# Performance work log

Measured on AMD Instinct MI355X. Metric: run time of the kernel, lower is better.

## Reference

```python
import jax, jax.numpy as jnp
import numpy as np

NHEAD = 8
HEAD_DIM = 64
WIN = 16  # attention_window w


def _window_index(T, w):
    # For shift slot i in [0, 2w], window[i, t] corresponds to source index t + (i - w).
    W = 2 * w + 1
    j = jnp.arange(T)[None, :] + (jnp.arange(W) - w)[:, None]  # [W, T]
    valid = (j >= 0) & (j < T)
    return jnp.clip(j, 0, T - 1), valid


def setup_inputs() -> dict:
    key = jax.random.key(0)
    ks = jax.random.split(key, 8)
    B, T, N, E = 2, 256, 8, 512
    scale = 1.0 / np.sqrt(E).astype(np.float32)
    return {
        "query": jax.random.normal(ks[0], (B, T, N, E), jnp.float32),
        "key": jax.random.normal(ks[1], (B, T, N, E), jnp.float32),
        "value": jax.random.normal(ks[2], (B, T, N, E), jnp.float32),
        "key_padding_mask": jnp.zeros((B, T, N), dtype=bool),
        "Wq": jax.random.normal(ks[3], (E, E), jnp.float32) * scale,
        "bq": jnp.zeros((E,), jnp.float32),
        "Wk": jax.random.normal(ks[4], (E, E), jnp.float32) * scale,
        "bk": jnp.zeros((E,), jnp.float32),
        "Wv": jax.random.normal(ks[5], (E, E), jnp.float32) * scale,
        "bv": jnp.zeros((E,), jnp.float32),
    }


def reference(query, key, value, key_padding_mask, Wq, bq, Wk, bk, Wv, bv):
    B, T, N, E = query.shape
    h, d, w = NHEAD, HEAD_DIM, WIN
    W = 2 * w + 1
    # linear projections (torch nn.Linear: x @ W.T + b)
    q = (query @ Wq.T + bq).reshape(B, T, N, h, d) / np.float32(np.sqrt(d))
    k = (key @ Wk.T + bk).reshape(B, T, N, h, d)
    v = (value @ Wv.T + bv).reshape(B, T, N, h, d)

    jc, valid = _window_index(T, w)           # [W, T], [W, T]
    vmask6 = valid[None, :, :, None, None, None]
    kwin = jnp.where(vmask6, k[:, jc], 0.0)   # [B, W, T, N, h, d]
    vwin = jnp.where(vmask6, v[:, jc], 0.0)   # [B, W, T, N, h, d]
    # mask: True = masked out (out-of-range stays True, like generate_mask)
    mwin = jnp.where(valid[None, :, :, None], key_padding_mask[:, jc], True)  # [B, W, T, N]

    logits = jnp.einsum('btnhd,bwtmhd->btnwmh', q, kwin)  # [B,T,N,W,N,h]
    mask = mwin.transpose(0, 2, 1, 3)[:, :, None, :, :, None]  # [B,T,1,W,N,1]
    logits = jnp.where(mask, -jnp.inf, logits)

    attn = jax.nn.softmax(logits.reshape(B, T, N, W * N, h), axis=-2)

    vw = vwin.transpose(0, 2, 1, 3, 4, 5).reshape(B, T, W * N, h, d)
    out = jnp.einsum('btnmh,btmhd->btnhd', attn, vw).reshape(B, T, N, E)
    return out, attn
```

## Files before the change

### kernel.cpp

```cpp
#include <hip/hip_runtime.h>
#include <hip/hip_bf16.h>

#define TSEQ 256
#define NBATCH 2
#define NAG 8
#define NH 8
#define HD 64
#define EE 512
#define WHALF 16
#define WW 33
#define WN 264

typedef __attribute__((ext_vector_type(8))) short short8;
typedef __attribute__((ext_vector_type(4))) short short4v;
typedef __attribute__((ext_vector_type(4))) float f32x4;
typedef _Float16 f16x8 __attribute__((ext_vector_type(8)));

static __device__ __forceinline__ unsigned short f2bf(float f) {
    unsigned int u = __float_as_uint(f);
    unsigned int r = (u + 0x7FFFu + ((u >> 16) & 1u)) >> 16;
    return (unsigned short)r;
}
static __device__ __forceinline__ unsigned int cvt_pk_bf16(float lo, float hi) {
    unsigned int r;
    asm("v_cvt_pk_bf16_f32 %0, %1, %2" : "=v"(r) : "v"(lo), "v"(hi));
    return r;
}
static __device__ __forceinline__ unsigned short f2h(float f) {
    _Float16 h = (_Float16)f;
    return __builtin_bit_cast(unsigned short, h);
}
static __device__ __forceinline__ float h2f(unsigned short u) {
    return (float)__builtin_bit_cast(_Float16, u);
}
static __device__ __forceinline__ f16x8 as_f16x8(short8 s) {
    return __builtin_bit_cast(f16x8, s);
}

__global__ __launch_bounds__(256)
void proj_mfma_kernel(const float* __restrict__ xq, const float* __restrict__ xk,
                      const float* __restrict__ xv,
                      const float* __restrict__ Wq, const float* __restrict__ Wk,
                      const float* __restrict__ Wv,
                      const float* __restrict__ bq, const float* __restrict__ bk,
                      const float* __restrict__ bv,
                      unsigned short* __restrict__ oq,
                      unsigned short* __restrict__ kswz,
                      unsigned short* __restrict__ vswz)
{
    __shared__ __align__(16) char LS[24576];
    char* As = LS;
    char* Bs = LS + 8192;

    const float* x; const float* W; const float* bias; float scale;
    const int z = blockIdx.z;
    if (z == 0)      { x = xq; W = Wq; bias = bq; scale = 0.125f; }
    else if (z == 1) { x = xk; W = Wk; bias = bk; scale = 1.0f; }
    else             { x = xv; W = Wv; bias = bv; scale = 1.0f; }

    const int tid  = threadIdx.x;
    const int lane = tid & 63;
    const int wid  = tid >> 6;
    const int i0 = blockIdx.x * 64;
    const int f0 = blockIdx.y * 128;
    const int wr = wid >> 1, wc = wid & 1;

    f32x4 acc[2][4];
    #pragma unroll
    for (int m = 0; m < 2; ++m)
        #pragma unroll
        for (int n = 0; n < 4; ++n)
            acc[m][n] = (f32x4){0.f, 0.f, 0.f, 0.f};

    for (int k0 = 0; k0 < EE; k0 += 64) {
        #pragma unroll
        for (int it = 0; it < 4; ++it) {
            const int tt  = tid + it * 256;
            const int row = tt >> 4, f4 = tt & 15;
            float4 v4 = *reinterpret_cast<const float4*>(x + (size_t)(i0 + row) * EE + k0 + f4 * 4);
            uint2 u;
            u.x = cvt_pk_bf16(v4.x, v4.y);
            u.y = cvt_pk_bf16(v4.z, v4.w);
            *(uint2*)(As + row * 128 + ((f4 * 8) ^ ((row & 7) << 4))) = u;
        }
        #pragma unroll
        for (int it = 0; it < 8; ++it) {
            const int tt  = tid + it * 256;
            const int row = tt >> 4, f4 = tt & 15;
            float4 v4 = *reinterpret_cast<const float4*>(W + (size_t)(f0 + row) * EE + k0 + f4 * 4);
            uint2 u;
            u.x = cvt_pk_bf16(v4.x, v4.y);
            u.y = cvt_pk_bf16(v4.z, v4.w);
            *(uint2*)(Bs + row * 128 + ((f4 * 8) ^ ((row & 7) << 4))) = u;
        }
        __syncthreads();

        #pragma unroll
        for (int ks = 0; ks < 2; ++ks) {
            short8 a[2], b[4];
            #pragma unroll
            for (int m = 0; m < 2; ++m) {
                const int row = wr * 32 + m * 16 + (lane & 15);
                a[m] = *(short8*)(As + row * 128 +
                                  ((ks * 64 + (lane >> 4) * 16) ^ ((row & 7) << 4)));
            }
            #pragma unroll
            for (int n = 0; n < 4; ++n) {
                const int row = wc * 64 + n * 16 + (lane & 15);
                b[n] = *(short8*)(Bs + row * 128 +
                                  ((ks * 64 + (lane >> 4) * 16) ^ ((row & 7) << 4)));
            }
            #pragma unroll
            for (int m = 0; m < 2; ++m)
                #pragma unroll
                for (int n = 0; n < 4; ++n)
                    acc[m][n] = __builtin_amdgcn_mfma_f32_16x16x32_bf16(a[m], b[n], acc[m][n], 0, 0, 0);
        }
        __syncthreads();
    }

    if (z == 0) {
        #pragma unroll
        for (int n = 0; n < 4; ++n) {
            const int col = f0 + wc * 64 + n * 16 + (lane & 15);
            const float bb = bias[col];
            #pragma unroll
            for (int m = 0; m < 2; ++m)
                #pragma unroll
                for (int rg = 0; rg < 4; ++rg) {
                    const int row = i0 + wr * 32 + m * 16 + (lane >> 4) * 4 + rg;
                    oq[(size_t)row * EE + col] = f2bf((acc[m][n][rg] + bb) * scale);
                }
        }
    } else if (z == 1) {
        unsigned short* ls16 = (unsigned short*)LS;
        const int b_ = i0 >> 11;
        const int c0 = i0 & 2047;
        const int h0 = f0 >> 6;
        #pragma unroll
        for (int n = 0; n < 4; ++n) {
            const int col = f0 + wc * 64 + n * 16 + (lane & 15);
            const int hl = (col >> 6) & 1;
            const int d  = col & 63;
            const float bb = bias[col];
            const int ib = (d >> 5) * 512 + ((d & 31) >> 3) * 128 + (d & 7);
            #pragma unroll
            for (int m = 0; m < 2; ++m) {
                #pragma unroll
                for (int rg = 0; rg < 4; ++rg) {
                    const int cl = wr * 32 + m * 16 + (lane >> 4) * 4 + rg;
                    ls16[(hl * 4 + (cl >> 4)) * 1024 + ib + (cl & 15) * 8] =
                        f2bf(acc[m][n][rg] + bb);
                }
            }
        }
        __syncthreads();
        #pragma unroll
        for (int it = 0; it < 4; ++it) {
            const int ci = tid + it * 256;
            const int hlfg = ci >> 7;
            const int hl = hlfg >> 2, fg = hlfg & 3;
            short8 v = *(short8*)(ls16 + ci * 8);
            *(short8*)(kswz + (size_t)(b_ * 8 + h0 + hl) * 131072 +
                       (size_t)((c0 >> 4) + fg) * 1024 + (ci & 127) * 8) = v;
        }
    } else {
        unsigned short* ls16 = (unsigned short*)LS;
        const int b_ = i0 >> 11;
        const int c0 = i0 & 2047;
        const int h0 = f0 >> 6;
        #pragma unroll
        for (int n = 0; n < 4; ++n) {
            const int col = f0 + wc * 64 + n * 16 + (lane & 15);
            const int hl = (col >> 6) & 1;
            const int d  = col & 63;
            const float bb = bias[col];
            const int ib = (d >> 4) * 512 + (d & 15) * 8;
            #pragma unroll
            for (int m = 0; m < 2; ++m) {
                #pragma unroll
                for (int rg = 0; rg < 4; ++rg) {
                    const int cl = wr * 32 + m * 16 + (lane >> 4) * 4 + rg;
                    ls16[(hl * 2 + (cl >> 5)) * 2048 + ib + ((cl >> 3) & 3) * 128 + (cl & 7)] =
                        f2h(acc[m][n][rg] + bb);
                }
            }
        }
        __syncthreads();
        #pragma unroll
        for (int it = 0; it < 4; ++it) {
            const int ci = tid + it * 256;
            const int hlch = ci >> 8;
            const int hl = hlch >> 1, ch = hlch & 1;
            short8 v = *(short8*)(ls16 + ci * 8);
            *(short8*)(vswz + (size_t)(b_ * 8 + h0 + hl) * 131072 +
                       (size_t)((c0 >> 5) + ch) * 2048 + (ci & 255) * 8) = v;
        }
    }
}

#define RSW  296
#define HS   2376
#define KM_OFF_B  (8 * HS * 2)
#define INV_OFF_B (KM_OFF_B + 288)
#define SMEM2_BYTES (INV_OFF_B + 256 + 32)

__global__ __launch_bounds__(512, 6)
void attn_fused_kernel(const unsigned short* __restrict__ qb,
                       const unsigned short* __restrict__ kswz,
                       const unsigned short* __restrict__ vswz,
                       const unsigned char* __restrict__ kpm,
                       float* __restrict__ out,
                       float* __restrict__ attn)
{
    extern __shared__ char smem[];
    unsigned short* P16 = (unsigned short*)smem;
    char*  km   = smem + KM_OFF_B;
    float* invs = (float*)(smem + INV_OFF_B);

    const int bid = blockIdx.x;
    const int lin = (bid & 7) * 64 + (bid >> 3);
    const int b   = lin >> 8;
    const int t   = lin & 255;
    const int jstart = (t - WHALF) & ~3;
    const int off8   = ((t - WHALF) - jstart) * 8;
    const int fgbase = jstart >> 1;
    const int kcbase = jstart >> 2;
    const int tid = threadIdx.x;
    const int lane = tid & 63;
    const int h    = tid >> 6;

    if (tid < 288) {
        const int j = jstart + (tid >> 3), m = tid & 7;
        const bool v = (j >= 0) && (j < TSEQ) && (j >= t - WHALF) && (j <= t + WHALF)
                       && (kpm[(b * TSEQ + j) * NAG + m] == 0);
        km[tid] = v ? 1 : 0;
    }

    {
        const int n = lane & 7;
        const unsigned short* qbase = qb + ((size_t)(b * TSEQ + t) * NAG + n) * EE + h * HD;
        short8 aq0 = *(const short8*)(qbase + (lane >> 4) * 8);
        short8 aq1 = *(const short8*)(qbase + 32 + (lane >> 4) * 8);
        const unsigned short* kbase = kswz + (size_t)(b * 8 + h) * 131072;
        unsigned short* Ph = P16 + h * HS;
        const int r0 = (lane >> 4) * 4;
        const int cl = lane & 15;

        auto kfrag = [&](int f, int half) -> const short8* {
            int fg = fgbase + f;
            fg = (fg < 0) ? 0 : ((fg > 127) ? 127 : fg);
            return (const short8*)(kbase + fg * 1024 + half * 512 + lane * 8);
        };

        short8 ka0[4], ka1[4];
        #pragma unroll
        for (int f = 0; f < 4; ++f) { ka0[f] = *kfrag(f, 0); ka1[f] = *kfrag(f, 1); }
        #pragma unroll
        for (int f = 0; f < 18; ++f) {
            f32x4 a = (f32x4){0.f, 0.f, 0.f, 0.f};
            a = __builtin_amdgcn_mfma_f32_16x16x32_bf16(aq0, ka0[f & 3], a, 0, 0, 0);
            a = __builtin_amdgcn_mfma_f32_16x16x32_bf16(aq1, ka1[f & 3], a, 0, 0, 0);
            if (f + 4 < 18) { ka0[f & 3] = *kfrag(f + 4, 0); ka1[f & 3] = *kfrag(f + 4, 1); }
            if (r0 < 8) {
                #pragma unroll
                for (int rg = 0; rg < 4; ++rg)
                    Ph[(r0 + rg) * RSW + f * 16 + cl] = f2h(a[rg]);
            }
        }
    }
    __syncthreads();

    {
        const int r = lane & 7, sub = lane >> 3;
        unsigned short* prow = P16 + h * HS + r * RSW;
        float mx = -INFINITY;
        #pragma unroll
        for (int i = 0; i < 36; ++i) {
            const int c = sub + 8 * i;
            if (km[c]) mx = fmaxf(mx, h2f(prow[c]));
        }
        mx = fmaxf(mx, __shfl_xor(mx, 8));
        mx = fmaxf(mx, __shfl_xor(mx, 16));
        mx = fmaxf(mx, __shfl_xor(mx, 32));
        float sum = 0.f;
        #pragma unroll
        for (int i = 0; i < 36; ++i) {
            const int c = sub + 8 * i;
            float p = 0.f;
            if (km[c]) p = __expf(h2f(prow[c]) - mx);
            prow[c] = f2h(p);
            sum += p;
        }
        sum += __shfl_xor(sum, 8);
        sum += __shfl_xor(sum, 16);
        sum += __shfl_xor(sum, 32);
        if (sub == 0) invs[h * 8 + r] = 1.f / sum;
    }
    __syncthreads();

    const unsigned short* vbase = vswz + (size_t)(b * 8 + h) * 131072;
    auto vfrag = [&](int ms, int df) -> const short8* {
        int kc = kcbase + ms;
        kc = (kc < 0) ? 0 : ((kc > 63) ? 63 : kc);
        return (const short8*)(vbase + kc * 2048 + df * 512 + lane * 8);
    };
    short8 vf[2][4];
    #pragma unroll
    for (int df = 0; df < 4; ++df) vf[0][df] = *vfrag(0, df);
    #pragma unroll
    for (int df = 0; df < 4; ++df) vf[1][df] = *vfrag(1, df);
    __builtin_amdgcn_sched_barrier(0);

    {
        float* abase = attn + (size_t)(b * TSEQ + t) * (NAG * WN * NH);
        #pragma unroll 3
        for (int q4 = tid; q4 < 4224; q4 += 512) {
            const int hh = q4 & 1;
            const int rw = q4 >> 1;
            const int n  = rw / WN;
            const int wm = rw - n * WN;
            const int h0 = hh * 4;
            const unsigned short* pp = P16 + h0 * HS + n * RSW + wm + off8;
            float4 v;
            v.x = h2f(pp[0])      * invs[(h0 + 0) * 8 + n];
            v.y = h2f(pp[HS])     * invs[(h0 + 1) * 8 + n];
            v.z = h2f(pp[2 * HS]) * invs[(h0 + 2) * 8 + n];
            v.w = h2f(pp[3 * HS]) * invs[(h0 + 3) * 8 + n];
            *(float4*)(abase + (size_t)q4 * 4) = v;
        }
    }

    {
        const unsigned short* arow = P16 + h * HS + (lane & 7) * RSW;
        f32x4 acc[4];
        #pragma unroll
        for (int df = 0; df < 4; ++df) acc[df] = (f32x4){0.f, 0.f, 0.f, 0.f};

        #pragma unroll
        for (int ms = 0; ms < 9; ++ms) {
            short8 afr = *(const short8*)(arow + ms * 32 + (lane >> 4) * 8);
            #pragma unroll
            for (int df = 0; df < 4; ++df)
                acc[df] = __builtin_amdgcn_mfma_f32_16x16x32_f16(
                    as_f16x8(afr), as_f16x8(vf[ms & 1][df]), acc[df], 0, 0, 0);
            if (ms + 2 < 9) {
                #pragma unroll
                for (int df = 0; df < 4; ++df) vf[ms & 1][df] = *vfrag(ms + 2, df);
            }
        }
        const int r0 = (lane >> 4) * 4;
        if (r0 < 8) {
            float iv[4];
            #pragma unroll
            for (int rg = 0; rg < 4; ++rg) iv[rg] = invs[h * 8 + r0 + rg];
            #pragma unroll
            for (int df = 0; df < 4; ++df) {
                const int d = df * 16 + (lane & 15);
                #pragma unroll
                for (int rg = 0; rg < 4; ++rg) {
                    const int n = r0 + rg;
                    out[((size_t)(b * TSEQ + t) * NAG + n) * EE + h * HD + d] = acc[df][rg] * iv[rg];
                }
            }
        }
    }
}

extern "C" void kernel_launch(void* const* d_in, const int* in_sizes, int n_in,
                              void* d_out, int out_size, void* d_ws, size_t ws_size,
                              hipStream_t stream) {
    const float* query = (const float*)d_in[0];
    const float* key   = (const float*)d_in[1];
    const float* value = (const float*)d_in[2];
    const unsigned char* kpm = (const unsigned char*)d_in[3];
    const float* Wq = (const float*)d_in[4];
    const float* bq = (const float*)d_in[5];
    const float* Wk = (const float*)d_in[6];
    const float* bk = (const float*)d_in[7];
    const float* Wv = (const float*)d_in[8];
    const float* bv = (const float*)d_in[9];

    float* out  = (float*)d_out;
    float* attn = out + (size_t)NBATCH * TSEQ * NAG * EE;

    unsigned short* qbf  = (unsigned short*)d_ws;
    unsigned short* kswz = qbf + (size_t)4096 * EE;
    unsigned short* vswz = kswz + (size_t)4096 * EE;

    dim3 gp(64, 4, 3);
    proj_mfma_kernel<<<gp, 256, 0, stream>>>(query, key, value,
                                             Wq, Wk, Wv, bq, bk, bv,
                                             qbf, kswz, vswz);

    (void)hipFuncSetAttribute((const void*)attn_fused_kernel,
                              hipFuncAttributeMaxDynamicSharedMemorySize, SMEM2_BYTES);
    attn_fused_kernel<<<512, 512, SMEM2_BYTES, stream>>>(qbf, kswz, vswz, kpm, out, attn);
}
```

Before: 45.23 us.

## Remap attention blocks to one head over four query positions

The fused attention kernel now gives each 256-thread block one head and four consecutive query positions, so the 16x16 MFMA tiles hold 32 real rows instead of 8 padded ones. Keys and values loaded for the shared window are reused across the four positions. The PV product is split across waves by output dimension. The cost is that the attn output store becomes a strided scalar write (stride NH floats) instead of contiguous float4 writes, and per-row masking logic is added.

```diff
diff --git a/kernel.cpp b/kernel.cpp
--- a/kernel.cpp
+++ b/kernel.cpp
@@ -199,13 +199,9 @@
     }
 }
 
-#define RSW  296
-#define HS   2376
-#define KM_OFF_B  (8 * HS * 2)
-#define INV_OFF_B (KM_OFF_B + 288)
-#define SMEM2_BYTES (INV_OFF_B + 256 + 32)
-
-__global__ __launch_bounds__(512, 6)
+#define RSW 296
+
+__global__ __launch_bounds__(256, 4)
 void attn_fused_kernel(const unsigned short* __restrict__ qb,
                        const unsigned short* __restrict__ kswz,
                        const unsigned short* __restrict__ vswz,
@@ -213,72 +209,82 @@
                        float* __restrict__ out,
                        float* __restrict__ attn)
 {
-    extern __shared__ char smem[];
-    unsigned short* P16 = (unsigned short*)smem;
-    char*  km   = smem + KM_OFF_B;
-    float* invs = (float*)(smem + INV_OFF_B);
-
-    const int bid = blockIdx.x;
-    const int lin = (bid & 7) * 64 + (bid >> 3);
-    const int b   = lin >> 8;
-    const int t   = lin & 255;
-    const int jstart = (t - WHALF) & ~3;
-    const int off8   = ((t - WHALF) - jstart) * 8;
+    __shared__ unsigned short P16[32 * RSW];
+    __shared__ char km[296];
+    __shared__ float invs[32];
+
+    const int bid  = blockIdx.x;
+    const int xcd  = bid & 7;
+    const int slot = bid >> 3;
+    const int h    = slot & 7;
+    const int g    = (slot >> 3) * 8 + xcd;
+    const int b    = g >> 6;
+    const int t0   = (g & 63) * 4;
+    const int jstart = t0 - WHALF;
     const int fgbase = jstart >> 1;
     const int kcbase = jstart >> 2;
-    const int tid = threadIdx.x;
+    const int tid  = threadIdx.x;
     const int lane = tid & 63;
-    const int h    = tid >> 6;
-
-    if (tid < 288) {
-        const int j = jstart + (tid >> 3), m = tid & 7;
-        const bool v = (j >= 0) && (j < TSEQ) && (j >= t - WHALF) && (j <= t + WHALF)
-                       && (kpm[(b * TSEQ + j) * NAG + m] == 0);
-        km[tid] = v ? 1 : 0;
+    const int w    = tid >> 6;
+
+    for (int i = tid; i < 288; i += 256) {
+        const int j = jstart + (i >> 3), m = i & 7;
+        km[i] = (j >= 0 && j < TSEQ && kpm[(b * TSEQ + j) * NAG + m] == 0) ? 1 : 0;
     }
 
     {
-        const int n = lane & 7;
-        const unsigned short* qbase = qb + ((size_t)(b * TSEQ + t) * NAG + n) * EE + h * HD;
-        short8 aq0 = *(const short8*)(qbase + (lane >> 4) * 8);
-        short8 aq1 = *(const short8*)(qbase + 32 + (lane >> 4) * 8);
+        const int row0 = lane & 15;
+        const int row1 = 16 + row0;
+        const int tq0 = t0 + (row0 >> 3), n0 = row0 & 7;
+        const int tq1 = t0 + (row1 >> 3), n1 = row1 & 7;
+        const unsigned short* qb0 = qb + ((size_t)(b * TSEQ + tq0) * NAG + n0) * EE + h * HD;
+        const unsigned short* qb1 = qb + ((size_t)(b * TSEQ + tq1) * NAG + n1) * EE + h * HD;
+        short8 aq[2][2];
+        aq[0][0] = *(const short8*)(qb0 + (lane >> 4) * 8);
+        aq[0][1] = *(const short8*)(qb0 + 32 + (lane >> 4) * 8);
+        aq[1][0] = *(const short8*)(qb1 + (lane >> 4) * 8);
+        aq[1][1] = *(const short8*)(qb1 + 32 + (lane >> 4) * 8);
+
         const unsigned short* kbase = kswz + (size_t)(b * 8 + h) * 131072;
-        unsigned short* Ph = P16 + h * HS;
         const int r0 = (lane >> 4) * 4;
         const int cl = lane & 15;
-
-        auto kfrag = [&](int f, int half) -> const short8* {
-            int fg = fgbase + f;
-            fg = (fg < 0) ? 0 : ((fg > 127) ? 127 : fg);
-            return (const short8*)(kbase + fg * 1024 + half * 512 + lane * 8);
-        };
-
-        short8 ka0[4], ka1[4];
-        #pragma unroll
-        for (int f = 0; f < 4; ++f) { ka0[f] = *kfrag(f, 0); ka1[f] = *kfrag(f, 1); }
-        #pragma unroll
-        for (int f = 0; f < 18; ++f) {
-            f32x4 a = (f32x4){0.f, 0.f, 0.f, 0.f};
-            a = __builtin_amdgcn_mfma_f32_16x16x32_bf16(aq0, ka0[f & 3], a, 0, 0, 0);
-            a = __builtin_amdgcn_mfma_f32_16x16x32_bf16(aq1, ka1[f & 3], a, 0, 0, 0);
-            if (f + 4 < 18) { ka0[f & 3] = *kfrag(f + 4, 0); ka1[f & 3] = *kfrag(f + 4, 1); }
-            if (r0 < 8) {
-                #pragma unroll
-                for (int rg = 0; rg < 4; ++rg)
-                    Ph[(r0 + rg) * RSW + f * 16 + cl] = f2h(a[rg]);
+        const int st  = (w < 2) ? w * 5 : 10 + (w - 2) * 4;
+        const int cnt = (w < 2) ? 5 : 4;
+
+        #pragma unroll
+        for (int k2 = 0; k2 < 5; ++k2) {
+            if (k2 < cnt) {
+                const int f = st + k2;
+                int fg = fgbase + f;
+                fg = (fg < 0) ? 0 : ((fg > 127) ? 127 : fg);
+                const unsigned short* kf = kbase + fg * 1024;
+                short8 ka0 = *(const short8*)(kf + lane * 8);
+                short8 ka1 = *(const short8*)(kf + 512 + lane * 8);
+                f32x4 a0 = (f32x4){0.f, 0.f, 0.f, 0.f};
+                f32x4 a1 = (f32x4){0.f, 0.f, 0.f, 0.f};
+                a0 = __builtin_amdgcn_mfma_f32_16x16x32_bf16(aq[0][0], ka0, a0, 0, 0, 0);
+                a0 = __builtin_amdgcn_mfma_f32_16x16x32_bf16(aq[0][1], ka1, a0, 0, 0, 0);
+                a1 = __builtin_amdgcn_mfma_f32_16x16x32_bf16(aq[1][0], ka0, a1, 0, 0, 0);
+                a1 = __builtin_amdgcn_mfma_f32_16x16x32_bf16(aq[1][1], ka1, a1, 0, 0, 0);
+                #pragma unroll
+                for (int rg = 0; rg < 4; ++rg) {
+                    P16[(r0 + rg) * RSW + f * 16 + cl]        = f2h(a0[rg]);
+                    P16[(16 + r0 + rg) * RSW + f * 16 + cl]   = f2h(a1[rg]);
+                }
             }
         }
     }
     __syncthreads();
 
     {
-        const int r = lane & 7, sub = lane >> 3;
-        unsigned short* prow = P16 + h * HS + r * RSW;
+        const int r = w * 8 + (lane & 7), sub = lane >> 3;
+        const int lo = w * 8;
+        unsigned short* prow = P16 + r * RSW;
         float mx = -INFINITY;
         #pragma unroll
         for (int i = 0; i < 36; ++i) {
             const int c = sub + 8 * i;
-            if (km[c]) mx = fmaxf(mx, h2f(prow[c]));
+            if (c >= lo && c < lo + WN && km[c]) mx = fmaxf(mx, h2f(prow[c]));
         }
         mx = fmaxf(mx, __shfl_xor(mx, 8));
         mx = fmaxf(mx, __shfl_xor(mx, 16));
@@ -288,81 +294,57 @@
         for (int i = 0; i < 36; ++i) {
             const int c = sub + 8 * i;
             float p = 0.f;
-            if (km[c]) p = __expf(h2f(prow[c]) - mx);
+            if (c >= lo && c < lo + WN && km[c]) p = __expf(h2f(prow[c]) - mx);
             prow[c] = f2h(p);
             sum += p;
         }
         sum += __shfl_xor(sum, 8);
         sum += __shfl_xor(sum, 16);
         sum += __shfl_xor(sum, 32);
-        if (sub == 0) invs[h * 8 + r] = 1.f / sum;
+        if (sub == 0) invs[r] = 1.f / sum;
     }
     __syncthreads();
 
-    const unsigned short* vbase = vswz + (size_t)(b * 8 + h) * 131072;
-    auto vfrag = [&](int ms, int df) -> const short8* {
-        int kc = kcbase + ms;
-        kc = (kc < 0) ? 0 : ((kc > 63) ? 63 : kc);
-        return (const short8*)(vbase + kc * 2048 + df * 512 + lane * 8);
-    };
-    short8 vf[2][4];
-    #pragma unroll
-    for (int df = 0; df < 4; ++df) vf[0][df] = *vfrag(0, df);
-    #pragma unroll
-    for (int df = 0; df < 4; ++df) vf[1][df] = *vfrag(1, df);
-    __builtin_amdgcn_sched_barrier(0);
-
     {
-        float* abase = attn + (size_t)(b * TSEQ + t) * (NAG * WN * NH);
+        float* abase = attn + (size_t)(b * TSEQ + t0) * (NAG * WN * NH) + h;
         #pragma unroll 3
-        for (int q4 = tid; q4 < 4224; q4 += 512) {
-            const int hh = q4 & 1;
-            const int rw = q4 >> 1;
-            const int n  = rw / WN;
-            const int wm = rw - n * WN;
-            const int h0 = hh * 4;
-            const unsigned short* pp = P16 + h0 * HS + n * RSW + wm + off8;
-            float4 v;
-            v.x = h2f(pp[0])      * invs[(h0 + 0) * 8 + n];
-            v.y = h2f(pp[HS])     * invs[(h0 + 1) * 8 + n];
-            v.z = h2f(pp[2 * HS]) * invs[(h0 + 2) * 8 + n];
-            v.w = h2f(pp[3 * HS]) * invs[(h0 + 3) * 8 + n];
-            *(float4*)(abase + (size_t)q4 * 4) = v;
+        for (int it = 0; it < 33; ++it) {
+            const int q4 = tid + it * 256;
+            const int th  = q4 / 2112;
+            const int rem = q4 - th * 2112;
+            const int n   = rem / WN;
+            const int wm  = rem - n * WN;
+            const int row = th * 8 + n;
+            const float v = h2f(P16[row * RSW + th * 8 + wm]) * invs[row];
+            abase[(size_t)(th * (NAG * WN) + n * WN + wm) * NH] = v;
         }
     }
 
     {
-        const unsigned short* arow = P16 + h * HS + (lane & 7) * RSW;
-        f32x4 acc[4];
-        #pragma unroll
-        for (int df = 0; df < 4; ++df) acc[df] = (f32x4){0.f, 0.f, 0.f, 0.f};
-
+        const unsigned short* vbase = vswz + (size_t)(b * 8 + h) * 131072 + w * 512;
+        const unsigned short* ar0 = P16 + (lane & 15) * RSW;
+        const unsigned short* ar1 = P16 + (16 + (lane & 15)) * RSW;
+        f32x4 acc0 = (f32x4){0.f, 0.f, 0.f, 0.f};
+        f32x4 acc1 = (f32x4){0.f, 0.f, 0.f, 0.f};
         #pragma unroll
         for (int ms = 0; ms < 9; ++ms) {
-            short8 afr = *(const short8*)(arow + ms * 32 + (lane >> 4) * 8);
-            #pragma unroll
-            for (int df = 0; df < 4; ++df)
-                acc[df] = __builtin_amdgcn_mfma_f32_16x16x32_f16(
-                    as_f16x8(afr), as_f16x8(vf[ms & 1][df]), acc[df], 0, 0, 0);
-            if (ms + 2 < 9) {
-                #pragma unroll
-                for (int df = 0; df < 4; ++df) vf[ms & 1][df] = *vfrag(ms + 2, df);
-            }
-        }
+            int kc = kcbase + ms;
+            kc = (kc < 0) ? 0 : ((kc > 63) ? 63 : kc);
+            short8 vf = *(const short8*)(vbase + (size_t)kc * 2048 + lane * 8);
+            short8 a0 = *(const short8*)(ar0 + ms * 32 + (lane >> 4) * 8);
+            short8 a1 = *(const short8*)(ar1 + ms * 32 + (lane >> 4) * 8);
+            acc0 = __builtin_amdgcn_mfma_f32_16x16x32_f16(as_f16x8(a0), as_f16x8(vf), acc0, 0, 0, 0);
+            acc1 = __builtin_amdgcn_mfma_f32_16x16x32_f16(as_f16x8(a1), as_f16x8(vf), acc1, 0, 0, 0);
+        }
+        const int d = w * 16 + (lane & 15);
         const int r0 = (lane >> 4) * 4;
-        if (r0 < 8) {
-            float iv[4];
-            #pragma unroll
-            for (int rg = 0; rg < 4; ++rg) iv[rg] = invs[h * 8 + r0 + rg];
-            #pragma unroll
-            for (int df = 0; df < 4; ++df) {
-                const int d = df * 16 + (lane & 15);
-                #pragma unroll
-                for (int rg = 0; rg < 4; ++rg) {
-                    const int n = r0 + rg;
-                    out[((size_t)(b * TSEQ + t) * NAG + n) * EE + h * HD + d] = acc[df][rg] * iv[rg];
-                }
-            }
+        #pragma unroll
+        for (int rg = 0; rg < 4; ++rg) {
+            const int ra = r0 + rg, rb = 16 + r0 + rg;
+            out[((size_t)(b * TSEQ + t0 + (ra >> 3)) * NAG + (ra & 7)) * EE + h * HD + d] =
+                acc0[rg] * invs[ra];
+            out[((size_t)(b * TSEQ + t0 + (rb >> 3)) * NAG + (rb & 7)) * EE + h * HD + d] =
+                acc1[rg] * invs[rb];
         }
     }
 }
@@ -393,7 +375,5 @@
                                              Wq, Wk, Wv, bq, bk, bv,
                                              qbf, kswz, vswz);
 
-    (void)hipFuncSetAttribute((const void*)attn_fused_kernel,
-                              hipFuncAttributeMaxDynamicSharedMemorySize, SMEM2_BYTES);
-    attn_fused_kernel<<<512, 512, SMEM2_BYTES, stream>>>(qbf, kswz, vswz, kpm, out, attn);
-}
+    attn_fused_kernel<<<1024, 256, 0, stream>>>(qbf, kswz, vswz, kpm, out, attn);
+}
```

Result: slower. 57.91 us (+28.0%).
